# Kernel tuning notes

Hardware: AMD Instinct MI355X
Metric: run time of the kernel (lower is better)

The kernel has to match this reference:

```python
import jax, jax.numpy as jnp
import numpy as np

B, N, F, H, K, L = 64, 96, 16, 128, 64, 3
CUTOFF, GAMMA = 10.0, 10.0


def setup_inputs() -> dict:
    key = jax.random.key(0)
    ks = jax.random.split(key, 20)
    X = jax.random.normal(ks[0], (B, N, F), dtype=jnp.float32)
    R = jax.random.normal(ks[1], (B, N, 3), dtype=jnp.float32) * 3.0
    # batch mask: -1 marks padded atoms (as in the original tf code)
    n_valid = jax.random.randint(ks[2], (B,), N // 2, N + 1)
    batch = jnp.where(jnp.arange(N)[None, :] < n_valid[:, None], 0, -1).astype(jnp.int32)

    def dense(k, fin, fout):
        s = 1.0 / np.sqrt(fin)
        return (jax.random.normal(k, (fin, fout), dtype=jnp.float32) * s,
                jnp.zeros((fout,), dtype=jnp.float32))

    We, be = dense(ks[3], F, H)
    Wrbf = jnp.stack([dense(jax.random.fold_in(ks[4], l), K, H)[0] for l in range(L)])
    brbf = jnp.zeros((L, H), dtype=jnp.float32)
    Wpair = jnp.stack([dense(jax.random.fold_in(ks[5], l), H, H)[0] for l in range(L)])
    bpair = jnp.zeros((L, H), dtype=jnp.float32)
    Wa1 = jnp.stack([dense(jax.random.fold_in(ks[6], l), H, H)[0] for l in range(L)])
    ba1 = jnp.zeros((L, H), dtype=jnp.float32)
    Wa2 = jnp.stack([dense(jax.random.fold_in(ks[7], l), H, H)[0] for l in range(L)])
    ba2 = jnp.zeros((L, H), dtype=jnp.float32)
    Wo1, bo1 = dense(ks[8], H, H)
    Wo2, bo2 = dense(ks[9], H, 1)
    return dict(X=X, R=R, batch=batch, We=We, be=be, Wrbf=Wrbf, brbf=brbf,
                Wpair=Wpair, bpair=bpair, Wa1=Wa1, ba1=ba1, Wa2=Wa2, ba2=ba2,
                Wo1=Wo1, bo1=bo1, Wo2=Wo2, bo2=bo2)


def reference(X, R, batch, We, be, Wrbf, brbf, Wpair, bpair, Wa1, ba1, Wa2, ba2, Wo1, bo1, Wo2, bo2):
    valid = (batch != -1)                             # [B,N]
    # all-pairs distances (self-pairs included, as in tf.meshgrid version)
    diff = R[:, :, None, :] - R[:, None, :, :]        # [B,N,N,3] send i, recv j
    d2 = jnp.sum(diff * diff, axis=-1)
    d = jnp.where(d2 > 0, jnp.sqrt(jnp.where(d2 > 0, d2, 1.0)), 0.0)  # safe norm
    centers = jnp.linspace(0.0, CUTOFF, K).astype(X.dtype)
    rbf = jnp.exp(-GAMMA * jnp.square(d[..., None] - centers))        # [B,N,N,K]
    h = X @ We + be                                    # [B,N,H]
    # edge mask: only edges between valid atoms contribute to the segment-sum
    emask = (valid[:, :, None] & valid[:, None, :])[..., None].astype(h.dtype)
    for l in range(L):
        msg = rbf @ Wrbf[l] + brbf[l]                  # [B,N,N,H]
        msg = msg @ Wpair[l] + bpair[l]
        agg = jnp.sum(msg * emask, axis=1)             # scatter-sum over senders -> [B,N,H]
        h = h + (jax.nn.silu(agg @ Wa1[l] + ba1[l]) @ Wa2[l] + ba2[l])
    o = jax.nn.silu(h @ Wo1 + bo1) @ Wo2 + bo2         # [B,N,1]
    vm = valid[..., None].astype(o.dtype)
    return jnp.sum(o * vm, axis=1) / jnp.sum(vm, axis=1)  # mean over valid atoms -> [B,1]
```

## Files before the change

kernel.cpp:

```cpp
#include <hip/hip_runtime.h>
#include <hip/hip_bf16.h>

#define BB 64
#define NN 96
#define FF 16
#define HH 128
#define KK 64
#define LL 3
#define CUTOFF_F 10.0f
#define GAMMA_F 10.0f

#define W3_BLOCKS 99
#define WA2_CP 12
#define WO1_CP 4
#define WE_CP 1
#define CNT_BLOCKS BB

#define SWZ(ch, k) ((ch) * 64 + ((k) ^ (((ch) & 7) << 3)))

__global__ __launch_bounds__(256) void pre_kernel(
    const float* __restrict__ Wrbf, const float* __restrict__ brbf,
    const float* __restrict__ Wpair, const float* __restrict__ bpair,
    const float* __restrict__ Wa1, const float* __restrict__ Wa2,
    const float* __restrict__ Wo1, const float* __restrict__ We,
    const int* __restrict__ batch,
    _Float16* __restrict__ W3c, float* __restrict__ c3,
    _Float16* __restrict__ Wa2c, _Float16* __restrict__ Wo1c,
    _Float16* __restrict__ Wec,
    float* __restrict__ cnt, float* __restrict__ out)
{
    const int bid = blockIdx.x;
    const int tid = threadIdx.x;
    if (bid < W3_BLOCKS) {
        __shared__ float sW2[2][HH];
        const int l    = bid / 33;
        const int r0   = (bid % 33) * 2;
        const int half = tid >> 7;
        const int h    = tid & 127;
        const int kk   = r0 + half;
        const bool active = (kk <= KK);
        if (active) {
            const float* Wp = Wpair + l * HH * HH + h;
            const float* arow;
            float acc;
            if (kk < KK) { arow = Wrbf + (l * KK + kk) * HH; acc = 0.f; }
            else         { arow = brbf + l * HH;             acc = bpair[l * HH + h]; }
            #pragma unroll 8
            for (int m = 0; m < HH; ++m) acc += arow[m] * Wp[m * HH];
            sW2[half][h] = acc;
        }
        __syncthreads();
        if (active) {
            const float* Wa = Wa1 + l * HH * HH + h;
            const float* row = sW2[half];
            float a3 = 0.f;
            #pragma unroll 8
            for (int m = 0; m < HH; ++m) a3 += row[m] * Wa[m * HH];
            if (kk < KK) W3c[l * 8192 + SWZ(h, kk)] = (_Float16)a3;
            else         c3[l * HH + h] = a3;
        }
    } else if (bid < W3_BLOCKS + WA2_CP) {
        int ci = bid - W3_BLOCKS;
        for (int e = tid; e < 4096; e += 256) {
            int E = ci * 4096 + e;
            int l = E / 16384, r = E % 16384;
            int k = r >> 7, ch = r & 127;
            Wa2c[l * 16384 + (k >> 6) * 8192 + SWZ(ch, k & 63)] = (_Float16)Wa2[E];
        }
    } else if (bid < W3_BLOCKS + WA2_CP + WO1_CP) {
        int ci = bid - W3_BLOCKS - WA2_CP;
        for (int e = tid; e < 4096; e += 256) {
            int E = ci * 4096 + e;
            int k = E >> 7, ch = E & 127;
            Wo1c[(k >> 6) * 8192 + SWZ(ch, k & 63)] = (_Float16)Wo1[E];
        }
    } else if (bid < W3_BLOCKS + WA2_CP + WO1_CP + WE_CP) {
        for (int e = tid; e < FF * HH; e += 256) {
            int f = e >> 7, ch = e & 127;
            Wec[ch * FF + f] = (_Float16)We[e];
        }
    } else {
        int b = bid - (W3_BLOCKS + WA2_CP + WO1_CP + WE_CP);
        __shared__ int c[4];
        bool v = (tid < NN) && (batch[b * NN + tid] != -1);
        unsigned long long m = __ballot(v);
        if ((tid & 63) == 0) c[tid >> 6] = __popcll(m);
        __syncthreads();
        if (tid == 0) {
            cnt[b] = (float)(c[0] + c[1] + c[2] + c[3]);
            out[b] = 0.f;
        }
    }
}

#define AT 12

typedef const __attribute__((address_space(1))) void* gp1_t;
typedef __attribute__((address_space(3))) void* lp3_t;
typedef _Float16 h8 __attribute__((ext_vector_type(8)));
typedef float f32x4 __attribute__((ext_vector_type(4)));

__device__ __forceinline__ void stage16(const _Float16* g, _Float16* lds, int tid)
{
    #pragma unroll
    for (int j = 0; j < 4; ++j) {
        const int u = j * 256 + tid;
        __builtin_amdgcn_global_load_lds((gp1_t)(g + (size_t)u * 8),
                                         (lp3_t)(lds + (size_t)u * 8), 16, 0, 0);
    }
}

#define BND(VM) do {                                                        \
    asm volatile("s_waitcnt vmcnt(" VM ") lgkmcnt(0)" ::: "memory");        \
    __builtin_amdgcn_s_barrier();                                           \
    __builtin_amdgcn_sched_barrier(0);                                      \
} while (0)

__device__ __forceinline__ float silu1(float v) { return v / (1.f + __expf(-v)); }

#define LDB(WC, CH, KB) (*(const h8*)&(WC)[(CH) * 64 + (((KB) + lg8) ^ (((CH) & 7) << 3))])
#define MFMA(A, B, C) __builtin_amdgcn_mfma_f32_16x16x32_f16((A), (B), (C), 0, 0, 0)

__global__ __launch_bounds__(256, 2) void chain_kernel(
    const float* __restrict__ X, const float* __restrict__ R,
    const float* __restrict__ be,
    const float* __restrict__ ba1, const float* __restrict__ ba2,
    const float* __restrict__ bo1, const float* __restrict__ Wo2,
    const float* __restrict__ bo2, const _Float16* __restrict__ W3c,
    const _Float16* __restrict__ Wa2c, const _Float16* __restrict__ Wo1c,
    const _Float16* __restrict__ Wec,
    const float* __restrict__ c3, const float* __restrict__ cnt,
    float* __restrict__ out)
{
    __shared__ __align__(16) _Float16 wb[4 * 8192];
    __shared__ __align__(16) _Float16 sST[16][72];
    __shared__ __align__(16) _Float16 thbuf[2 * 16 * 136];
    __shared__ __align__(16) _Float16 sXh[16][32];
    __shared__ float po[4][16];

    _Float16 (*tbT)[136] = (_Float16(*)[136])thbuf;
    _Float16 (*hbT)[136] = (_Float16(*)[136])(thbuf + 16 * 136);
    float* sD  = (float*)thbuf;
    float* sRf = sD + AT * NN;

    const int tid  = threadIdx.x;
    const int lane = tid & 63;
    const int wv   = tid >> 6;
    const int l15  = lane & 15;
    const int lg   = lane >> 4;
    const int lg8  = lg * 8;
    const int lg4  = lg * 4;
    const int a0   = blockIdx.x * AT;
    const int b    = a0 / NN;
    const int lbase = a0 - b * NN;
    const float cb = cnt[b];
    const int nv   = (int)cb;

    const int chA = 32 * wv + l15;
    const int chB = chA + 16;

    for (int t = tid; t < NN * 3; t += 256) sRf[t] = R[b * NN * 3 + t];
    for (int t = tid; t < 512; t += 256) {
        int row = t >> 5, col = t & 31;
        float v = (row < AT && col < FF) ? X[(a0 + row) * FF + col] : 0.f;
        sXh[row][col] = (_Float16)v;
    }
    __syncthreads();

    for (int e = tid; e < AT * NN; e += 256) {
        int j = e / NN, i = e - j * NN;
        float dx = sRf[i * 3 + 0] - sRf[(lbase + j) * 3 + 0];
        float dy = sRf[i * 3 + 1] - sRf[(lbase + j) * 3 + 1];
        float dz = sRf[i * 3 + 2] - sRf[(lbase + j) * 3 + 2];
        sD[e] = sqrtf(dx * dx + dy * dy + dz * dz);
    }
    __syncthreads();

    const float be_a = be[chA], be_b = be[chB];
    const float bo1_a = bo1[chA], bo1_b = bo1[chB];
    const float wo2_a = Wo2[chA], wo2_b = Wo2[chB];
    const float bo2R = bo2[0];
    const float c3_0a = c3[chA], c3_0b = c3[chB];
    const float c3_1a = c3[HH + chA], c3_1b = c3[HH + chB];
    const float c3_2a = c3[2 * HH + chA], c3_2b = c3[2 * HH + chB];
    const float ba1_0a = ba1[chA], ba1_0b = ba1[chB];
    const float ba1_1a = ba1[HH + chA], ba1_1b = ba1[HH + chB];
    const float ba1_2a = ba1[2 * HH + chA], ba1_2b = ba1[2 * HH + chB];
    const float ba2_0a = ba2[chA], ba2_0b = ba2[chB];
    const float ba2_1a = ba2[HH + chA], ba2_1b = ba2[HH + chB];
    const float ba2_2a = ba2[2 * HH + chA], ba2_2b = ba2[2 * HH + chB];
    h8 weA = (h8)(_Float16)0.f, weB = (h8)(_Float16)0.f;
    if (lg < 2) {
        weA = *(const h8*)&Wec[chA * FF + lg8];
        weB = *(const h8*)&Wec[chB * FF + lg8];
    }

    stage16(W3c,          wb + 0 * 8192, tid);
    stage16(Wa2c,         wb + 1 * 8192, tid);
    stage16(Wa2c + 8192,  wb + 2 * 8192, tid);
    stage16(W3c + 8192,   wb + 3 * 8192, tid);

    {
        const float ck = (float)lane * (CUTOFF_F / (float)(KK - 1));
        #pragma unroll
        for (int r = 0; r < 3; ++r) {
            int j = 3 * wv + r;
            if (lbase + j >= nv) { sST[j][lane] = (_Float16)0.f; continue; }
            const float* Dr = sD + j * NN;
            float acc = 0.f;
            for (int i = 0; i < nv; ++i) {
                float u = Dr[i] - ck;
                acc += __expf(-GAMMA_F * u * u);
            }
            sST[j][lane] = (_Float16)acc;
        }
        sST[12 + wv][lane] = (_Float16)0.f;
    }

    f32x4 hA, hB;
    {
        f32x4 z = {0.f, 0.f, 0.f, 0.f};
        h8 xa = *(const h8*)&sXh[l15][lg8];
        hA = MFMA(xa, weA, z);
        hB = MFMA(xa, weB, z);
        #pragma unroll
        for (int r = 0; r < 4; ++r) { hA[r] += be_a; hB[r] += be_b; }
    }

    BND("12");

    #pragma unroll 1
    for (int l = 0; l < LL; ++l) {
        const float c3a  = (l == 0) ? c3_0a  : (l == 1) ? c3_1a  : c3_2a;
        const float c3b  = (l == 0) ? c3_0b  : (l == 1) ? c3_1b  : c3_2b;
        const float ba1a = (l == 0) ? ba1_0a : (l == 1) ? ba1_1a : ba1_2a;
        const float ba1b = (l == 0) ? ba1_0b : (l == 1) ? ba1_1b : ba1_2b;
        const float ba2a = (l == 0) ? ba2_0a : (l == 1) ? ba2_1a : ba2_2a;
        const float ba2b = (l == 0) ? ba2_0b : (l == 1) ? ba2_1b : ba2_2b;
        const int c_g1 = 3 * l;

        f32x4 accA, accB;
        {
            f32x4 z = {0.f, 0.f, 0.f, 0.f};
            const _Float16* wc = wb + (size_t)(c_g1 & 3) * 8192;
            h8 s0 = *(const h8*)&sST[l15][lg8];
            h8 s1 = *(const h8*)&sST[l15][32 + lg8];
            accA = MFMA(s0, LDB(wc, chA, 0), z);
            accA = MFMA(s1, LDB(wc, chA, 32), accA);
            accB = MFMA(s0, LDB(wc, chB, 0), z);
            accB = MFMA(s1, LDB(wc, chB, 32), accB);
        }
        {
            float biasA = cb * c3a + ba1a, biasB = cb * c3b + ba1b;
            #pragma unroll
            for (int r = 0; r < 4; ++r) {
                tbT[lg4 + r][chA] = (_Float16)silu1(accA[r] + biasA);
                tbT[lg4 + r][chB] = (_Float16)silu1(accB[r] + biasB);
            }
        }
        BND("8");
        { int i = c_g1 + 4; if (i < 11) {
            const _Float16* p = (i >= 9) ? (Wo1c + (size_t)(i - 9) * 8192)
                : ((i % 3) == 0 ? (W3c + (size_t)(i / 3) * 8192)
                                : (Wa2c + (size_t)(i / 3) * 16384 + (size_t)(i % 3 - 1) * 8192));
            stage16(p, wb + (size_t)(i & 3) * 8192, tid); } }

        {
            const _Float16* wc = wb + (size_t)((c_g1 + 1) & 3) * 8192;
            h8 t0 = *(const h8*)&tbT[l15][lg8];
            h8 t1 = *(const h8*)&tbT[l15][32 + lg8];
            hA = MFMA(t0, LDB(wc, chA, 0), hA);
            hA = MFMA(t1, LDB(wc, chA, 32), hA);
            hB = MFMA(t0, LDB(wc, chB, 0), hB);
            hB = MFMA(t1, LDB(wc, chB, 32), hB);
        }
        BND("8");
        { int i = c_g1 + 5; if (i < 11) {
            const _Float16* p = (i >= 9) ? (Wo1c + (size_t)(i - 9) * 8192)
                : ((i % 3) == 0 ? (W3c + (size_t)(i / 3) * 8192)
                                : (Wa2c + (size_t)(i / 3) * 16384 + (size_t)(i % 3 - 1) * 8192));
            stage16(p, wb + (size_t)(i & 3) * 8192, tid); } }

        {
            const _Float16* wc = wb + (size_t)((c_g1 + 2) & 3) * 8192;
            h8 t2 = *(const h8*)&tbT[l15][64 + lg8];
            h8 t3 = *(const h8*)&tbT[l15][96 + lg8];
            hA = MFMA(t2, LDB(wc, chA, 0), hA);
            hA = MFMA(t3, LDB(wc, chA, 32), hA);
            hB = MFMA(t2, LDB(wc, chB, 0), hB);
            hB = MFMA(t3, LDB(wc, chB, 32), hB);
        }
        #pragma unroll
        for (int r = 0; r < 4; ++r) { hA[r] += ba2a; hB[r] += ba2b; }
        if (l == LL - 1) {
            #pragma unroll
            for (int r = 0; r < 4; ++r) {
                hbT[lg4 + r][chA] = (_Float16)hA[r];
                hbT[lg4 + r][chB] = (_Float16)hB[r];
            }
        }
        BND("8");
        { int i = c_g1 + 6; if (i < 11) {
            const _Float16* p = (i >= 9) ? (Wo1c + (size_t)(i - 9) * 8192)
                : ((i % 3) == 0 ? (W3c + (size_t)(i / 3) * 8192)
                                : (Wa2c + (size_t)(i / 3) * 16384 + (size_t)(i % 3 - 1) * 8192));
            stage16(p, wb + (size_t)(i & 3) * 8192, tid); } }
    }

    BND("4");
    f32x4 oA, oB;
    {
        f32x4 z = {0.f, 0.f, 0.f, 0.f};
        const _Float16* wc = wb + 1 * 8192;
        h8 a0 = *(const h8*)&hbT[l15][lg8];
        h8 a1 = *(const h8*)&hbT[l15][32 + lg8];
        oA = MFMA(a0, LDB(wc, chA, 0), z);
        oA = MFMA(a1, LDB(wc, chA, 32), oA);
        oB = MFMA(a0, LDB(wc, chB, 0), z);
        oB = MFMA(a1, LDB(wc, chB, 32), oB);
    }
    BND("0");
    {
        const _Float16* wc = wb + 2 * 8192;
        h8 a2 = *(const h8*)&hbT[l15][64 + lg8];
        h8 a3 = *(const h8*)&hbT[l15][96 + lg8];
        oA = MFMA(a2, LDB(wc, chA, 0), oA);
        oA = MFMA(a3, LDB(wc, chA, 32), oA);
        oB = MFMA(a2, LDB(wc, chB, 0), oB);
        oB = MFMA(a3, LDB(wc, chB, 32), oB);
    }

    float p[4];
    #pragma unroll
    for (int r = 0; r < 4; ++r)
        p[r] = silu1(oA[r] + bo1_a) * wo2_a + silu1(oB[r] + bo1_b) * wo2_b;
    #pragma unroll
    for (int r = 0; r < 4; ++r) {
        p[r] += __shfl_xor(p[r], 1);
        p[r] += __shfl_xor(p[r], 2);
        p[r] += __shfl_xor(p[r], 4);
        p[r] += __shfl_xor(p[r], 8);
    }
    if (l15 == 0) {
        #pragma unroll
        for (int r = 0; r < 4; ++r) po[wv][lg4 + r] = p[r];
    }
    __syncthreads();
    if (tid == 0) {
        float sum = 0.f;
        #pragma unroll
        for (int j = 0; j < AT; ++j) {
            if (lbase + j < nv)
                sum += po[0][j] + po[1][j] + po[2][j] + po[3][j] + bo2R;
        }
        atomicAdd(out + b, sum / cb);
    }
}

extern "C" void kernel_launch(void* const* d_in, const int* in_sizes, int n_in,
                              void* d_out, int out_size, void* d_ws, size_t ws_size,
                              hipStream_t stream) {
    const float* X     = (const float*)d_in[0];
    const float* R     = (const float*)d_in[1];
    const int*   batch = (const int*)  d_in[2];
    const float* We    = (const float*)d_in[3];
    const float* be    = (const float*)d_in[4];
    const float* Wrbf  = (const float*)d_in[5];
    const float* brbf  = (const float*)d_in[6];
    const float* Wpair = (const float*)d_in[7];
    const float* bpair = (const float*)d_in[8];
    const float* Wa1   = (const float*)d_in[9];
    const float* ba1   = (const float*)d_in[10];
    const float* Wa2   = (const float*)d_in[11];
    const float* ba2   = (const float*)d_in[12];
    const float* Wo1   = (const float*)d_in[13];
    const float* bo1   = (const float*)d_in[14];
    const float* Wo2   = (const float*)d_in[15];
    const float* bo2   = (const float*)d_in[16];

    char* wsb = (char*)d_ws;
    _Float16* W3c  = (_Float16*)wsb;
    _Float16* Wa2c = (_Float16*)(wsb + 49152);
    _Float16* Wo1c = (_Float16*)(wsb + 147456);
    _Float16* Wec  = (_Float16*)(wsb + 180224);
    float*    c3   = (float*)(wsb + 184320);
    float*    cnt  = (float*)(wsb + 185856);
    float*    out  = (float*)d_out;

    hipLaunchKernelGGL(pre_kernel,
                       dim3(W3_BLOCKS + WA2_CP + WO1_CP + WE_CP + CNT_BLOCKS), dim3(256),
                       0, stream, Wrbf, brbf, Wpair, bpair, Wa1, Wa2, Wo1, We, batch,
                       W3c, c3, Wa2c, Wo1c, Wec, cnt, out);
    hipLaunchKernelGGL(chain_kernel, dim3(BB * NN / AT), dim3(256), 0, stream,
                       X, R, be, ba1, ba2, bo1, Wo2, bo2,
                       W3c, Wa2c, Wo1c, Wec, c3, cnt, out);
}
```

Before: 30.69 us.

## Fuse weight-prep and main chain into one cooperative kernel with grid sync

Merges the weight-preprocessing kernel into the main kernel, launched cooperatively. The first blocks fold Wrbf, Wpair and Wa1 into W3 (each K row now split across both thread halves) and convert the other weights to swizzled fp16. Every block counts its own valid atoms and computes its RBF sums before a grid-wide sync, so that work overlaps the weight preparation. This removes one kernel launch and the inter-kernel gap, at the cost of a grid barrier and a grid size that must fit co-resident on the device.

```diff
diff --git a/kernel.cpp b/kernel.cpp
--- a/kernel.cpp
+++ b/kernel.cpp
@@ -1,5 +1,8 @@
 #include <hip/hip_runtime.h>
 #include <hip/hip_bf16.h>
+#include <hip/hip_cooperative_groups.h>
+
+namespace cg = cooperative_groups;
 
 #define BB 64
 #define NN 96
@@ -10,90 +13,9 @@
 #define CUTOFF_F 10.0f
 #define GAMMA_F 10.0f
 
-#define W3_BLOCKS 99
-#define WA2_CP 12
-#define WO1_CP 4
-#define WE_CP 1
-#define CNT_BLOCKS BB
+#define AT 12
 
 #define SWZ(ch, k) ((ch) * 64 + ((k) ^ (((ch) & 7) << 3)))
-
-__global__ __launch_bounds__(256) void pre_kernel(
-    const float* __restrict__ Wrbf, const float* __restrict__ brbf,
-    const float* __restrict__ Wpair, const float* __restrict__ bpair,
-    const float* __restrict__ Wa1, const float* __restrict__ Wa2,
-    const float* __restrict__ Wo1, const float* __restrict__ We,
-    const int* __restrict__ batch,
-    _Float16* __restrict__ W3c, float* __restrict__ c3,
-    _Float16* __restrict__ Wa2c, _Float16* __restrict__ Wo1c,
-    _Float16* __restrict__ Wec,
-    float* __restrict__ cnt, float* __restrict__ out)
-{
-    const int bid = blockIdx.x;
-    const int tid = threadIdx.x;
-    if (bid < W3_BLOCKS) {
-        __shared__ float sW2[2][HH];
-        const int l    = bid / 33;
-        const int r0   = (bid % 33) * 2;
-        const int half = tid >> 7;
-        const int h    = tid & 127;
-        const int kk   = r0 + half;
-        const bool active = (kk <= KK);
-        if (active) {
-            const float* Wp = Wpair + l * HH * HH + h;
-            const float* arow;
-            float acc;
-            if (kk < KK) { arow = Wrbf + (l * KK + kk) * HH; acc = 0.f; }
-            else         { arow = brbf + l * HH;             acc = bpair[l * HH + h]; }
-            #pragma unroll 8
-            for (int m = 0; m < HH; ++m) acc += arow[m] * Wp[m * HH];
-            sW2[half][h] = acc;
-        }
-        __syncthreads();
-        if (active) {
-            const float* Wa = Wa1 + l * HH * HH + h;
-            const float* row = sW2[half];
-            float a3 = 0.f;
-            #pragma unroll 8
-            for (int m = 0; m < HH; ++m) a3 += row[m] * Wa[m * HH];
-            if (kk < KK) W3c[l * 8192 + SWZ(h, kk)] = (_Float16)a3;
-            else         c3[l * HH + h] = a3;
-        }
-    } else if (bid < W3_BLOCKS + WA2_CP) {
-        int ci = bid - W3_BLOCKS;
-        for (int e = tid; e < 4096; e += 256) {
-            int E = ci * 4096 + e;
-            int l = E / 16384, r = E % 16384;
-            int k = r >> 7, ch = r & 127;
-            Wa2c[l * 16384 + (k >> 6) * 8192 + SWZ(ch, k & 63)] = (_Float16)Wa2[E];
-        }
-    } else if (bid < W3_BLOCKS + WA2_CP + WO1_CP) {
-        int ci = bid - W3_BLOCKS - WA2_CP;
-        for (int e = tid; e < 4096; e += 256) {
-            int E = ci * 4096 + e;
-            int k = E >> 7, ch = E & 127;
-            Wo1c[(k >> 6) * 8192 + SWZ(ch, k & 63)] = (_Float16)Wo1[E];
-        }
-    } else if (bid < W3_BLOCKS + WA2_CP + WO1_CP + WE_CP) {
-        for (int e = tid; e < FF * HH; e += 256) {
-            int f = e >> 7, ch = e & 127;
-            Wec[ch * FF + f] = (_Float16)We[e];
-        }
-    } else {
-        int b = bid - (W3_BLOCKS + WA2_CP + WO1_CP + WE_CP);
-        __shared__ int c[4];
-        bool v = (tid < NN) && (batch[b * NN + tid] != -1);
-        unsigned long long m = __ballot(v);
-        if ((tid & 63) == 0) c[tid >> 6] = __popcll(m);
-        __syncthreads();
-        if (tid == 0) {
-            cnt[b] = (float)(c[0] + c[1] + c[2] + c[3]);
-            out[b] = 0.f;
-        }
-    }
-}
-
-#define AT 12
 
 typedef const __attribute__((address_space(1))) void* gp1_t;
 typedef __attribute__((address_space(3))) void* lp3_t;
@@ -121,22 +43,27 @@
 #define LDB(WC, CH, KB) (*(const h8*)&(WC)[(CH) * 64 + (((KB) + lg8) ^ (((CH) & 7) << 3))])
 #define MFMA(A, B, C) __builtin_amdgcn_mfma_f32_16x16x32_f16((A), (B), (C), 0, 0, 0)
 
-__global__ __launch_bounds__(256, 2) void chain_kernel(
+__global__ __launch_bounds__(256, 2) void fused_kernel(
     const float* __restrict__ X, const float* __restrict__ R,
-    const float* __restrict__ be,
-    const float* __restrict__ ba1, const float* __restrict__ ba2,
-    const float* __restrict__ bo1, const float* __restrict__ Wo2,
-    const float* __restrict__ bo2, const _Float16* __restrict__ W3c,
-    const _Float16* __restrict__ Wa2c, const _Float16* __restrict__ Wo1c,
-    const _Float16* __restrict__ Wec,
-    const float* __restrict__ c3, const float* __restrict__ cnt,
-    float* __restrict__ out)
+    const int* __restrict__ batch,
+    const float* __restrict__ We, const float* __restrict__ be,
+    const float* __restrict__ Wrbf, const float* __restrict__ brbf,
+    const float* __restrict__ Wpair, const float* __restrict__ bpair,
+    const float* __restrict__ Wa1, const float* __restrict__ ba1,
+    const float* __restrict__ Wa2, const float* __restrict__ ba2,
+    const float* __restrict__ Wo1, const float* __restrict__ bo1,
+    const float* __restrict__ Wo2, const float* __restrict__ bo2,
+    _Float16* __restrict__ W3c, float* __restrict__ c3,
+    _Float16* __restrict__ Wa2c, _Float16* __restrict__ Wo1c,
+    _Float16* __restrict__ Wec, float* __restrict__ out)
 {
     __shared__ __align__(16) _Float16 wb[4 * 8192];
     __shared__ __align__(16) _Float16 sST[16][72];
     __shared__ __align__(16) _Float16 thbuf[2 * 16 * 136];
     __shared__ __align__(16) _Float16 sXh[16][32];
     __shared__ float po[4][16];
+    __shared__ float preW[3][HH];
+    __shared__ int cpop[4];
 
     _Float16 (*tbT)[136] = (_Float16(*)[136])thbuf;
     _Float16 (*hbT)[136] = (_Float16(*)[136])(thbuf + 16 * 136);
@@ -150,20 +77,74 @@
     const int lg   = lane >> 4;
     const int lg8  = lg * 8;
     const int lg4  = lg * 4;
-    const int a0   = blockIdx.x * AT;
+    const int bid  = blockIdx.x;
+    const int a0   = bid * AT;
     const int b    = a0 / NN;
     const int lbase = a0 - b * NN;
-    const float cb = cnt[b];
-    const int nv   = (int)cb;
 
     const int chA = 32 * wv + l15;
     const int chB = chA + 16;
 
+    {
+        bool v = (tid < NN) && (batch[b * NN + tid] != -1);
+        unsigned long long mb = __ballot(v);
+        if ((tid & 63) == 0) cpop[wv] = __popcll(mb);
+    }
     for (int t = tid; t < NN * 3; t += 256) sRf[t] = R[b * NN * 3 + t];
     for (int t = tid; t < 512; t += 256) {
         int row = t >> 5, col = t & 31;
         float v = (row < AT && col < FF) ? X[(a0 + row) * FF + col] : 0.f;
         sXh[row][col] = (_Float16)v;
+    }
+    __syncthreads();
+    const int nv = cpop[0] + cpop[1] + cpop[2] + cpop[3];
+    const float cb = (float)nv;
+
+    if (bid < 195) {
+        const int l = bid / 65, kk = bid % 65;
+        const int kh = tid >> 7, h = tid & 127;
+        const float* arow = (kk < KK) ? (Wrbf + (l * KK + kk) * HH) : (brbf + l * HH);
+        const float* Wp = Wpair + l * HH * HH + h;
+        float part = 0.f;
+        #pragma unroll 8
+        for (int m = 64 * kh; m < 64 * kh + 64; ++m) part += arow[m] * Wp[m * HH];
+        preW[kh][h] = part;
+        __syncthreads();
+        if (kh == 0)
+            preW[2][h] = preW[0][h] + preW[1][h] + ((kk == KK) ? bpair[l * HH + h] : 0.f);
+        __syncthreads();
+        const float* Wa = Wa1 + l * HH * HH + h;
+        float p2 = 0.f;
+        #pragma unroll 8
+        for (int m = 64 * kh; m < 64 * kh + 64; ++m) p2 += preW[2][m] * Wa[m * HH];
+        preW[kh][h] = p2;
+        __syncthreads();
+        if (kh == 0) {
+            float a3 = preW[0][h] + preW[1][h];
+            if (kk < KK) W3c[l * 8192 + SWZ(h, kk)] = (_Float16)a3;
+            else         c3[l * HH + h] = a3;
+        }
+    } else if (bid < 207) {
+        int ci = bid - 195;
+        for (int e = tid; e < 4096; e += 256) {
+            int E = ci * 4096 + e;
+            int l = E / 16384, r = E % 16384;
+            int k = r >> 7, ch = r & 127;
+            Wa2c[l * 16384 + (k >> 6) * 8192 + SWZ(ch, k & 63)] = (_Float16)Wa2[E];
+        }
+    } else if (bid < 211) {
+        int ci = bid - 207;
+        for (int e = tid; e < 4096; e += 256) {
+            int E = ci * 4096 + e;
+            int k = E >> 7, ch = E & 127;
+            Wo1c[(k >> 6) * 8192 + SWZ(ch, k & 63)] = (_Float16)Wo1[E];
+        }
+    } else if (bid == 211) {
+        for (int e = tid; e < FF * HH; e += 256) {
+            int f = e >> 7, ch = e & 127;
+            Wec[ch * FF + f] = (_Float16)We[e];
+        }
+        if (tid < BB) out[tid] = 0.f;
     }
     __syncthreads();
 
@@ -175,6 +156,25 @@
         sD[e] = sqrtf(dx * dx + dy * dy + dz * dz);
     }
     __syncthreads();
+
+    {
+        const float ck = (float)lane * (CUTOFF_F / (float)(KK - 1));
+        #pragma unroll
+        for (int r = 0; r < 3; ++r) {
+            int j = 3 * wv + r;
+            if (lbase + j >= nv) { sST[j][lane] = (_Float16)0.f; continue; }
+            const float* Dr = sD + j * NN;
+            float acc = 0.f;
+            for (int i = 0; i < nv; ++i) {
+                float u = Dr[i] - ck;
+                acc += __expf(-GAMMA_F * u * u);
+            }
+            sST[j][lane] = (_Float16)acc;
+        }
+        sST[12 + wv][lane] = (_Float16)0.f;
+    }
+
+    cg::this_grid().sync();
 
     const float be_a = be[chA], be_b = be[chB];
     const float bo1_a = bo1[chA], bo1_b = bo1[chB];
@@ -200,23 +200,6 @@
     stage16(Wa2c + 8192,  wb + 2 * 8192, tid);
     stage16(W3c + 8192,   wb + 3 * 8192, tid);
 
-    {
-        const float ck = (float)lane * (CUTOFF_F / (float)(KK - 1));
-        #pragma unroll
-        for (int r = 0; r < 3; ++r) {
-            int j = 3 * wv + r;
-            if (lbase + j >= nv) { sST[j][lane] = (_Float16)0.f; continue; }
-            const float* Dr = sD + j * NN;
-            float acc = 0.f;
-            for (int i = 0; i < nv; ++i) {
-                float u = Dr[i] - ck;
-                acc += __expf(-GAMMA_F * u * u);
-            }
-            sST[j][lane] = (_Float16)acc;
-        }
-        sST[12 + wv][lane] = (_Float16)0.f;
-    }
-
     f32x4 hA, hB;
     {
         f32x4 z = {0.f, 0.f, 0.f, 0.f};
@@ -312,22 +295,22 @@
     {
         f32x4 z = {0.f, 0.f, 0.f, 0.f};
         const _Float16* wc = wb + 1 * 8192;
-        h8 a0 = *(const h8*)&hbT[l15][lg8];
-        h8 a1 = *(const h8*)&hbT[l15][32 + lg8];
-        oA = MFMA(a0, LDB(wc, chA, 0), z);
-        oA = MFMA(a1, LDB(wc, chA, 32), oA);
-        oB = MFMA(a0, LDB(wc, chB, 0), z);
-        oB = MFMA(a1, LDB(wc, chB, 32), oB);
+        h8 a0f = *(const h8*)&hbT[l15][lg8];
+        h8 a1f = *(const h8*)&hbT[l15][32 + lg8];
+        oA = MFMA(a0f, LDB(wc, chA, 0), z);
+        oA = MFMA(a1f, LDB(wc, chA, 32), oA);
+        oB = MFMA(a0f, LDB(wc, chB, 0), z);
+        oB = MFMA(a1f, LDB(wc, chB, 32), oB);
     }
     BND("0");
     {
         const _Float16* wc = wb + 2 * 8192;
-        h8 a2 = *(const h8*)&hbT[l15][64 + lg8];
-        h8 a3 = *(const h8*)&hbT[l15][96 + lg8];
-        oA = MFMA(a2, LDB(wc, chA, 0), oA);
-        oA = MFMA(a3, LDB(wc, chA, 32), oA);
-        oB = MFMA(a2, LDB(wc, chB, 0), oB);
-        oB = MFMA(a3, LDB(wc, chB, 32), oB);
+        h8 a2f = *(const h8*)&hbT[l15][64 + lg8];
+        h8 a3f = *(const h8*)&hbT[l15][96 + lg8];
+        oA = MFMA(a2f, LDB(wc, chA, 0), oA);
+        oA = MFMA(a3f, LDB(wc, chA, 32), oA);
+        oB = MFMA(a2f, LDB(wc, chB, 0), oB);
+        oB = MFMA(a3f, LDB(wc, chB, 32), oB);
     }
 
     float p[4];
@@ -384,14 +367,16 @@
     _Float16* Wo1c = (_Float16*)(wsb + 147456);
     _Float16* Wec  = (_Float16*)(wsb + 180224);
     float*    c3   = (float*)(wsb + 184320);
-    float*    cnt  = (float*)(wsb + 185856);
     float*    out  = (float*)d_out;
 
-    hipLaunchKernelGGL(pre_kernel,
-                       dim3(W3_BLOCKS + WA2_CP + WO1_CP + WE_CP + CNT_BLOCKS), dim3(256),
-                       0, stream, Wrbf, brbf, Wpair, bpair, Wa1, Wa2, Wo1, We, batch,
-                       W3c, c3, Wa2c, Wo1c, Wec, cnt, out);
-    hipLaunchKernelGGL(chain_kernel, dim3(BB * NN / AT), dim3(256), 0, stream,
-                       X, R, be, ba1, ba2, bo1, Wo2, bo2,
-                       W3c, Wa2c, Wo1c, Wec, c3, cnt, out);
+    void* kargs[] = {
+        (void*)&X, (void*)&R, (void*)&batch, (void*)&We, (void*)&be,
+        (void*)&Wrbf, (void*)&brbf, (void*)&Wpair, (void*)&bpair,
+        (void*)&Wa1, (void*)&ba1, (void*)&Wa2, (void*)&ba2,
+        (void*)&Wo1, (void*)&bo1, (void*)&Wo2, (void*)&bo2,
+        (void*)&W3c, (void*)&c3, (void*)&Wa2c, (void*)&Wo1c,
+        (void*)&Wec, (void*)&out
+    };
+    hipLaunchCooperativeKernel((const void*)fused_kernel,
+                               dim3(BB * NN / AT), dim3(256), kargs, 0, stream);
 }
```

Result: slower. 97.86 us (+218.8%).

## Compute valid-atom count in chain kernel and merge per-layer weight staging barriers

Applied to the files above, without the earlier changes.

Removes the per-batch count blocks from the preprocessing kernel. Each chain block now counts valid atoms itself with a ballot and popcount, reusing the existing barrier. In the layer loop, the two Wa2 half-chunk MFMA phases become one phase behind a single barrier, and the next two chunk loads are issued together. The output Wo1 step likewise waits once for both chunks. This cuts barriers and pre-kernel work, but overlaps less of the weight loads with compute and may create LDS buffer-reuse hazards in the 4-slot ring.

```diff
diff --git a/kernel.cpp b/kernel.cpp
--- a/kernel.cpp
+++ b/kernel.cpp
@@ -14,7 +14,6 @@
 #define WA2_CP 12
 #define WO1_CP 4
 #define WE_CP 1
-#define CNT_BLOCKS BB
 
 #define SWZ(ch, k) ((ch) * 64 + ((k) ^ (((ch) & 7) << 3)))
 
@@ -23,11 +22,9 @@
     const float* __restrict__ Wpair, const float* __restrict__ bpair,
     const float* __restrict__ Wa1, const float* __restrict__ Wa2,
     const float* __restrict__ Wo1, const float* __restrict__ We,
-    const int* __restrict__ batch,
     _Float16* __restrict__ W3c, float* __restrict__ c3,
     _Float16* __restrict__ Wa2c, _Float16* __restrict__ Wo1c,
-    _Float16* __restrict__ Wec,
-    float* __restrict__ cnt, float* __restrict__ out)
+    _Float16* __restrict__ Wec, float* __restrict__ out)
 {
     const int bid = blockIdx.x;
     const int tid = threadIdx.x;
@@ -74,22 +71,12 @@
             int k = E >> 7, ch = E & 127;
             Wo1c[(k >> 6) * 8192 + SWZ(ch, k & 63)] = (_Float16)Wo1[E];
         }
-    } else if (bid < W3_BLOCKS + WA2_CP + WO1_CP + WE_CP) {
+    } else {
         for (int e = tid; e < FF * HH; e += 256) {
             int f = e >> 7, ch = e & 127;
             Wec[ch * FF + f] = (_Float16)We[e];
         }
-    } else {
-        int b = bid - (W3_BLOCKS + WA2_CP + WO1_CP + WE_CP);
-        __shared__ int c[4];
-        bool v = (tid < NN) && (batch[b * NN + tid] != -1);
-        unsigned long long m = __ballot(v);
-        if ((tid & 63) == 0) c[tid >> 6] = __popcll(m);
-        __syncthreads();
-        if (tid == 0) {
-            cnt[b] = (float)(c[0] + c[1] + c[2] + c[3]);
-            out[b] = 0.f;
-        }
+        if (tid < BB) out[tid] = 0.f;
     }
 }
 
@@ -118,25 +105,33 @@
 
 __device__ __forceinline__ float silu1(float v) { return v / (1.f + __expf(-v)); }
 
+__device__ __forceinline__ const _Float16* chunk_src(int i, const _Float16* W3c,
+    const _Float16* Wa2c, const _Float16* Wo1c)
+{
+    if (i >= 9) return Wo1c + (size_t)(i - 9) * 8192;
+    if (i % 3 == 0) return W3c + (size_t)(i / 3) * 8192;
+    return Wa2c + (size_t)(i / 3) * 16384 + (size_t)(i % 3 - 1) * 8192;
+}
+
 #define LDB(WC, CH, KB) (*(const h8*)&(WC)[(CH) * 64 + (((KB) + lg8) ^ (((CH) & 7) << 3))])
 #define MFMA(A, B, C) __builtin_amdgcn_mfma_f32_16x16x32_f16((A), (B), (C), 0, 0, 0)
 
 __global__ __launch_bounds__(256, 2) void chain_kernel(
     const float* __restrict__ X, const float* __restrict__ R,
-    const float* __restrict__ be,
+    const int* __restrict__ batch, const float* __restrict__ be,
     const float* __restrict__ ba1, const float* __restrict__ ba2,
     const float* __restrict__ bo1, const float* __restrict__ Wo2,
     const float* __restrict__ bo2, const _Float16* __restrict__ W3c,
     const _Float16* __restrict__ Wa2c, const _Float16* __restrict__ Wo1c,
     const _Float16* __restrict__ Wec,
-    const float* __restrict__ c3, const float* __restrict__ cnt,
-    float* __restrict__ out)
+    const float* __restrict__ c3, float* __restrict__ out)
 {
     __shared__ __align__(16) _Float16 wb[4 * 8192];
     __shared__ __align__(16) _Float16 sST[16][72];
     __shared__ __align__(16) _Float16 thbuf[2 * 16 * 136];
     __shared__ __align__(16) _Float16 sXh[16][32];
     __shared__ float po[4][16];
+    __shared__ int cpop[4];
 
     _Float16 (*tbT)[136] = (_Float16(*)[136])thbuf;
     _Float16 (*hbT)[136] = (_Float16(*)[136])(thbuf + 16 * 136);
@@ -150,15 +145,19 @@
     const int lg   = lane >> 4;
     const int lg8  = lg * 8;
     const int lg4  = lg * 4;
-    const int a0   = blockIdx.x * AT;
+    const int bid  = blockIdx.x;
+    const int a0   = bid * AT;
     const int b    = a0 / NN;
     const int lbase = a0 - b * NN;
-    const float cb = cnt[b];
-    const int nv   = (int)cb;
 
     const int chA = 32 * wv + l15;
     const int chB = chA + 16;
 
+    {
+        bool v = (tid < NN) && (batch[b * NN + tid] != -1);
+        unsigned long long mb = __ballot(v);
+        if ((tid & 63) == 0) cpop[wv] = __popcll(mb);
+    }
     for (int t = tid; t < NN * 3; t += 256) sRf[t] = R[b * NN * 3 + t];
     for (int t = tid; t < 512; t += 256) {
         int row = t >> 5, col = t & 31;
@@ -166,6 +165,8 @@
         sXh[row][col] = (_Float16)v;
     }
     __syncthreads();
+    const int nv = cpop[0] + cpop[1] + cpop[2] + cpop[3];
+    const float cb = (float)nv;
 
     for (int e = tid; e < AT * NN; e += 256) {
         int j = e / NN, i = e - j * NN;
@@ -258,37 +259,25 @@
                 tbT[lg4 + r][chB] = (_Float16)silu1(accB[r] + biasB);
             }
         }
-        BND("8");
-        { int i = c_g1 + 4; if (i < 11) {
-            const _Float16* p = (i >= 9) ? (Wo1c + (size_t)(i - 9) * 8192)
-                : ((i % 3) == 0 ? (W3c + (size_t)(i / 3) * 8192)
-                                : (Wa2c + (size_t)(i / 3) * 16384 + (size_t)(i % 3 - 1) * 8192));
-            stage16(p, wb + (size_t)(i & 3) * 8192, tid); } }
+        BND("4");
+        { int i = c_g1 + 4; if (i < 11)
+            stage16(chunk_src(i, W3c, Wa2c, Wo1c), wb + (size_t)(i & 3) * 8192, tid); }
 
         {
-            const _Float16* wc = wb + (size_t)((c_g1 + 1) & 3) * 8192;
+            const _Float16* wcA = wb + (size_t)((c_g1 + 1) & 3) * 8192;
+            const _Float16* wcB2 = wb + (size_t)((c_g1 + 2) & 3) * 8192;
             h8 t0 = *(const h8*)&tbT[l15][lg8];
             h8 t1 = *(const h8*)&tbT[l15][32 + lg8];
-            hA = MFMA(t0, LDB(wc, chA, 0), hA);
-            hA = MFMA(t1, LDB(wc, chA, 32), hA);
-            hB = MFMA(t0, LDB(wc, chB, 0), hB);
-            hB = MFMA(t1, LDB(wc, chB, 32), hB);
-        }
-        BND("8");
-        { int i = c_g1 + 5; if (i < 11) {
-            const _Float16* p = (i >= 9) ? (Wo1c + (size_t)(i - 9) * 8192)
-                : ((i % 3) == 0 ? (W3c + (size_t)(i / 3) * 8192)
-                                : (Wa2c + (size_t)(i / 3) * 16384 + (size_t)(i % 3 - 1) * 8192));
-            stage16(p, wb + (size_t)(i & 3) * 8192, tid); } }
-
-        {
-            const _Float16* wc = wb + (size_t)((c_g1 + 2) & 3) * 8192;
             h8 t2 = *(const h8*)&tbT[l15][64 + lg8];
             h8 t3 = *(const h8*)&tbT[l15][96 + lg8];
-            hA = MFMA(t2, LDB(wc, chA, 0), hA);
-            hA = MFMA(t3, LDB(wc, chA, 32), hA);
-            hB = MFMA(t2, LDB(wc, chB, 0), hB);
-            hB = MFMA(t3, LDB(wc, chB, 32), hB);
+            hA = MFMA(t0, LDB(wcA, chA, 0), hA);
+            hA = MFMA(t1, LDB(wcA, chA, 32), hA);
+            hB = MFMA(t0, LDB(wcA, chB, 0), hB);
+            hB = MFMA(t1, LDB(wcA, chB, 32), hB);
+            hA = MFMA(t2, LDB(wcB2, chA, 0), hA);
+            hA = MFMA(t3, LDB(wcB2, chA, 32), hA);
+            hB = MFMA(t2, LDB(wcB2, chB, 0), hB);
+            hB = MFMA(t3, LDB(wcB2, chB, 32), hB);
         }
         #pragma unroll
         for (int r = 0; r < 4; ++r) { hA[r] += ba2a; hB[r] += ba2b; }
@@ -299,35 +288,33 @@
                 hbT[lg4 + r][chB] = (_Float16)hB[r];
             }
         }
-        BND("8");
-        { int i = c_g1 + 6; if (i < 11) {
-            const _Float16* p = (i >= 9) ? (Wo1c + (size_t)(i - 9) * 8192)
-                : ((i % 3) == 0 ? (W3c + (size_t)(i / 3) * 8192)
-                                : (Wa2c + (size_t)(i / 3) * 16384 + (size_t)(i % 3 - 1) * 8192));
-            stage16(p, wb + (size_t)(i & 3) * 8192, tid); } }
-    }
-
-    BND("4");
+        if (l < LL - 1) {
+            BND("4");
+            { int i = c_g1 + 5; if (i < 11)
+                stage16(chunk_src(i, W3c, Wa2c, Wo1c), wb + (size_t)(i & 3) * 8192, tid); }
+            { int i = c_g1 + 6; if (i < 11)
+                stage16(chunk_src(i, W3c, Wa2c, Wo1c), wb + (size_t)(i & 3) * 8192, tid); }
+        }
+    }
+
+    BND("0");
     f32x4 oA, oB;
     {
         f32x4 z = {0.f, 0.f, 0.f, 0.f};
-        const _Float16* wc = wb + 1 * 8192;
-        h8 a0 = *(const h8*)&hbT[l15][lg8];
-        h8 a1 = *(const h8*)&hbT[l15][32 + lg8];
-        oA = MFMA(a0, LDB(wc, chA, 0), z);
-        oA = MFMA(a1, LDB(wc, chA, 32), oA);
-        oB = MFMA(a0, LDB(wc, chB, 0), z);
-        oB = MFMA(a1, LDB(wc, chB, 32), oB);
-    }
-    BND("0");
-    {
-        const _Float16* wc = wb + 2 * 8192;
-        h8 a2 = *(const h8*)&hbT[l15][64 + lg8];
-        h8 a3 = *(const h8*)&hbT[l15][96 + lg8];
-        oA = MFMA(a2, LDB(wc, chA, 0), oA);
-        oA = MFMA(a3, LDB(wc, chA, 32), oA);
-        oB = MFMA(a2, LDB(wc, chB, 0), oB);
-        oB = MFMA(a3, LDB(wc, chB, 32), oB);
+        const _Float16* wc9 = wb + 1 * 8192;
+        const _Float16* wc10 = wb + 2 * 8192;
+        h8 a0f = *(const h8*)&hbT[l15][lg8];
+        h8 a1f = *(const h8*)&hbT[l15][32 + lg8];
+        h8 a2f = *(const h8*)&hbT[l15][64 + lg8];
+        h8 a3f = *(const h8*)&hbT[l15][96 + lg8];
+        oA = MFMA(a0f, LDB(wc9, chA, 0), z);
+        oA = MFMA(a1f, LDB(wc9, chA, 32), oA);
+        oB = MFMA(a0f, LDB(wc9, chB, 0), z);
+        oB = MFMA(a1f, LDB(wc9, chB, 32), oB);
+        oA = MFMA(a2f, LDB(wc10, chA, 0), oA);
+        oA = MFMA(a3f, LDB(wc10, chA, 32), oA);
+        oB = MFMA(a2f, LDB(wc10, chB, 0), oB);
+        oB = MFMA(a3f, LDB(wc10, chB, 32), oB);
     }
 
     float p[4];
@@ -384,14 +371,13 @@
     _Float16* Wo1c = (_Float16*)(wsb + 147456);
     _Float16* Wec  = (_Float16*)(wsb + 180224);
     float*    c3   = (float*)(wsb + 184320);
-    float*    cnt  = (float*)(wsb + 185856);
     float*    out  = (float*)d_out;
 
     hipLaunchKernelGGL(pre_kernel,
-                       dim3(W3_BLOCKS + WA2_CP + WO1_CP + WE_CP + CNT_BLOCKS), dim3(256),
-                       0, stream, Wrbf, brbf, Wpair, bpair, Wa1, Wa2, Wo1, We, batch,
-                       W3c, c3, Wa2c, Wo1c, Wec, cnt, out);
+                       dim3(W3_BLOCKS + WA2_CP + WO1_CP + WE_CP), dim3(256),
+                       0, stream, Wrbf, brbf, Wpair, bpair, Wa1, Wa2, Wo1, We,
+                       W3c, c3, Wa2c, Wo1c, Wec, out);
     hipLaunchKernelGGL(chain_kernel, dim3(BB * NN / AT), dim3(256), 0, stream,
-                       X, R, be, ba1, ba2, bo1, Wo2, bo2,
-                       W3c, Wa2c, Wo1c, Wec, c3, cnt, out);
-}
+                       X, R, batch, be, ba1, ba2, bo1, Wo2, bo2,
+                       W3c, Wa2c, Wo1c, Wec, c3, out);
+}
```

Measured after the change: 30.94 us. Within noise of the previous version (+0.8%).
